# Kernel optimization log

Measured on AMD Instinct MI355X. Metric: run time of the kernel, lower is better.

## Reference

```python
import jax, jax.numpy as jnp
import numpy as np

EPS = 1e-5


def conv3x3(x, w, b):
    # x [B,C,H,W], w [O,C,3,3], stride 1, pad 1
    y = jax.lax.conv_general_dilated(x, w, (1, 1), ((1, 1), (1, 1)),
                                     dimension_numbers=('NCHW', 'OIHW', 'NCHW'))
    return y + b[None, :, None, None]


def bilinear_gather(x, py, px):
    # x [B,C,H,W]; sampling locations py,px [B,K,H,W] -> [B,C,K,H,W]
    # Zero padding outside the image (matches deform_conv CUDA semantics:
    # out-of-bound corner values contribute 0).
    B, C, H, W = x.shape
    K = py.shape[1]
    x_flat = x.reshape(B, C, H * W)
    y0 = jnp.floor(py)
    x0 = jnp.floor(px)
    out = jnp.zeros((B, C, K, H, W), x.dtype)
    for dy in (0.0, 1.0):
        for dx in (0.0, 1.0):
            yi = y0 + dy
            xi = x0 + dx
            wgt = (1.0 - jnp.abs(py - yi)) * (1.0 - jnp.abs(px - xi))  # [B,K,H,W]
            valid = (yi >= 0) & (yi <= H - 1) & (xi >= 0) & (xi <= W - 1)
            idx = (jnp.clip(yi, 0, H - 1).astype(jnp.int32) * W
                   + jnp.clip(xi, 0, W - 1).astype(jnp.int32)).reshape(B, -1)
            vals = jax.vmap(lambda xf, i: xf[:, i])(x_flat, idx)  # [B,C,K*H*W]
            out = out + (wgt * valid)[:, None] * vals.reshape(B, C, K, H, W)
    return out


def setup_inputs() -> dict:
    key = jax.random.key(0)
    k1, k2, k3 = jax.random.split(key, 3)
    B, C, O, H, W = 4, 64, 64, 128, 128
    x = jax.random.normal(k1, (B, C, H, W), jnp.float32)
    # offset predictor: small init so predicted offsets are modest (realistic)
    off_w = 0.01 * jax.random.normal(k2, (18, C, 3, 3), jnp.float32)
    off_b = jnp.zeros((18,), jnp.float32)
    dc_w = jax.random.normal(k3, (O, C, 3, 3), jnp.float32) / np.sqrt(C * 9)
    dc_b = jnp.zeros((O,), jnp.float32)
    gamma = jnp.ones((O,), jnp.float32)
    beta = jnp.zeros((O,), jnp.float32)
    return {"x": x, "off_w": off_w, "off_b": off_b, "dc_w": dc_w,
            "dc_b": dc_b, "gamma": gamma, "beta": beta}


def reference(x, off_w, off_b, dc_w, dc_b, gamma, beta):
    B, C, H, W = x.shape
    O = dc_w.shape[0]
    K = 9  # 3x3 kernel
    offset = conv3x3(x, off_w, off_b)              # [B,18,H,W]
    off = offset.reshape(B, K, 2, H, W)            # (dy,dx) per kernel tap, row-major
    dyo, dxo = off[:, :, 0], off[:, :, 1]          # [B,K,H,W]
    k = (jnp.arange(3) - 1).astype(x.dtype)        # kernel taps {-1,0,1}
    kgy = jnp.repeat(k, 3)                         # [9] row-major y offsets
    kgx = jnp.tile(k, 3)                           # [9] row-major x offsets
    hh = jnp.arange(H, dtype=x.dtype)
    ww = jnp.arange(W, dtype=x.dtype)
    # stride 1, pad 1: base point = out_pos - 1 + tap; pad is folded into kgy/kgx
    py = hh[None, None, :, None] + kgy[None, :, None, None] + dyo
    px = ww[None, None, None, :] + kgx[None, :, None, None] + dxo
    sampled = bilinear_gather(x, py, px)           # [B,C,K,H,W]
    y = jnp.einsum('ock,bckhw->bohw', dc_w.reshape(O, C, K), sampled)
    y = y + dc_b[None, :, None, None]
    # BatchNorm2d (training mode: biased batch statistics)
    mu = y.mean(axis=(0, 2, 3), keepdims=True)
    var = y.var(axis=(0, 2, 3), keepdims=True)
    yn = (y - mu) * jax.lax.rsqrt(var + EPS)
    return jax.nn.relu(yn * gamma[None, :, None, None] + beta[None, :, None, None])
```

## Files before the change

kernel.cpp:

```cpp
#include <hip/hip_runtime.h>

#define HH 128
#define WW 128
#define HWSZ (HH * WW)
#define CC 64
#define OO 64
#define BB 4
#define NOFF 18
#define KK 576

#define WS_BG     0
#define WS_BGO    18432
#define WS_SUMS   27648
#define WS_SUMSQ  27712
#define WS_YBUF   27776

typedef __attribute__((ext_vector_type(8))) short short8;
typedef __attribute__((ext_vector_type(4))) int int4v;
typedef __attribute__((ext_vector_type(2))) unsigned int uint2v;
typedef __attribute__((ext_vector_type(4))) float f32x4;

__device__ inline unsigned bf16rne(float f) {
  unsigned u = __float_as_uint(f);
  u += 0x7fff + ((u >> 16) & 1);
  return u >> 16;
}

__global__ __launch_bounds__(256) void prep_kernel(
    const float* __restrict__ x, const float* __restrict__ off_w,
    const float* __restrict__ dc_w, unsigned int* __restrict__ xTu,
    int* __restrict__ Bg, int* __restrict__ Bgo, float* __restrict__ sums) {
  int bid = blockIdx.x;
  if (bid < BB * HH) {
    __shared__ float T[CC][WW + 1];
    int b = bid >> 7, h = bid & 127;
    int tw = threadIdx.x & 127, th = threadIdx.x >> 7;
    const float* xp = x + (size_t)b * CC * HWSZ + h * WW;
#pragma unroll 8
    for (int i = 0; i < 32; ++i) {
      int c = i * 2 + th;
      T[c][tw] = xp[c * HWSZ + tw];
    }
    __syncthreads();
    int c2 = threadIdx.x & 31, wq = threadIdx.x >> 5;
    unsigned int* op = xTu + ((size_t)(b * HH + h) * WW) * 32;
#pragma unroll 8
    for (int i = 0; i < 16; ++i) {
      int w = i * 8 + wq;
      unsigned pk = bf16rne(T[2 * c2][w]) | (bf16rne(T[2 * c2 + 1][w]) << 16);
      op[w * 32 + c2] = pk;
    }
  } else {
    int pb = bid - BB * HH;
    int tid = pb * 256 + threadIdx.x;
    int stride = 64 * 256;
    for (int i = tid; i < 72 * 64 * 4; i += stride) {
      int j = i & 3, o = (i >> 2) & 63, g = i >> 8;
      int k2 = g * 4 + j, t = k2 >> 5, jj = k2 & 31;
      unsigned lo = bf16rne(dc_w[o * KK + (2 * jj) * 9 + t]);
      unsigned hi = bf16rne(dc_w[o * KK + (2 * jj + 1) * 9 + t]);
      Bg[i] = (int)(lo | (hi << 16));
    }
    for (int i = tid; i < 72 * 32 * 4; i += stride) {
      int j = i & 3, o = (i >> 2) & 31, g = i >> 7;
      int k2 = g * 4 + j, t = k2 >> 5, jj = k2 & 31;
      unsigned pk = 0;
      if (o < NOFF) {
        unsigned lo = bf16rne(off_w[o * KK + (2 * jj) * 9 + t]);
        unsigned hi = bf16rne(off_w[o * KK + (2 * jj + 1) * 9 + t]);
        pk = lo | (hi << 16);
      }
      Bgo[i] = (int)pk;
    }
    if (tid < 128) sums[tid] = 0.0f;
  }
}

#define G_ISSUE(i, T, PH)                                                     \
  int4v m##i, da##i, db##i, dcv##i, dd##i;                                    \
  {                                                                           \
    m##i = *(const int4v*)&Mw[(((PH) * 8 + p8) * 9 + (T)) * 4];               \
    unsigned x_ = (unsigned)m##i.x, y_ = (unsigned)m##i.y;                    \
    da##i  = *(const int4v*)&xbu[(x_ & 0xffffu) * 32 + cq4];                  \
    db##i  = *(const int4v*)&xbu[(x_ >> 16) * 32 + cq4];                      \
    dcv##i = *(const int4v*)&xbu[(y_ & 0xffffu) * 32 + cq4];                  \
    dd##i  = *(const int4v*)&xbu[(y_ >> 16) * 32 + cq4];                      \
  }

#define G_BLEND(i, T, PH)                                                     \
  {                                                                           \
    float w00_ = __uint_as_float(((unsigned)m##i.z) << 16);                   \
    float w01_ = __uint_as_float(((unsigned)m##i.z) & 0xffff0000u);           \
    float w10_ = __uint_as_float(((unsigned)m##i.w) << 16);                   \
    float w11_ = __uint_as_float(((unsigned)m##i.w) & 0xffff0000u);           \
    int4v pk_;                                                                \
    _Pragma("unroll")                                                         \
    for (int j = 0; j < 4; ++j) {                                             \
      float slo_ = w00_ * __uint_as_float(((unsigned)da##i[j]) << 16);        \
      slo_ = fmaf(w01_, __uint_as_float(((unsigned)db##i[j]) << 16), slo_);   \
      slo_ = fmaf(w10_, __uint_as_float(((unsigned)dcv##i[j]) << 16), slo_);  \
      slo_ = fmaf(w11_, __uint_as_float(((unsigned)dd##i[j]) << 16), slo_);   \
      float shi_ = w00_ * __uint_as_float(((unsigned)da##i[j]) & 0xffff0000u);\
      shi_ = fmaf(w01_, __uint_as_float(((unsigned)db##i[j]) & 0xffff0000u), shi_);\
      shi_ = fmaf(w10_, __uint_as_float(((unsigned)dcv##i[j]) & 0xffff0000u), shi_);\
      shi_ = fmaf(w11_, __uint_as_float(((unsigned)dd##i[j]) & 0xffff0000u), shi_);\
      pk_[j] = (int)__builtin_amdgcn_perm(__float_as_uint(shi_) + 0x8000u,    \
                                          __float_as_uint(slo_) + 0x8000u,    \
                                          0x07060302u);                       \
    }                                                                         \
    *(int4v*)&A[abase + ((T) & 1) * 544 + ((PH) * 8 + p8) * 34 + cq4] = pk_;  \
  }

#define MFMA_TAP(T)                                                           \
  {                                                                           \
    _Pragma("unroll")                                                         \
    for (int kk2 = 0; kk2 < 2; ++kk2) {                                       \
      int4v av = *(const int4v*)&A[abase + ((T) & 1) * 544 + n16 * 34 + kk2 * 16 + q * 4]; \
      short8 af = __builtin_bit_cast(short8, av);                             \
      int g = (T) * 8 + kk2 * 4 + q;                                          \
      _Pragma("unroll")                                                       \
      for (int nt = 0; nt < 4; ++nt) {                                        \
        int4v bv = *(const int4v*)&Bg[(g * 64 + nt * 16 + n16) * 4];          \
        short8 bfr = __builtin_bit_cast(short8, bv);                          \
        acc[nt] = __builtin_amdgcn_mfma_f32_16x16x32_bf16(af, bfr, acc[nt], 0, 0, 0); \
      }                                                                       \
    }                                                                         \
  }

__global__ __launch_bounds__(256, 6) void fused_kernel(
    const unsigned int* __restrict__ xTu, const int* __restrict__ Bg,
    const int* __restrict__ Bgo, const float* __restrict__ off_b,
    const float* __restrict__ dc_b, unsigned int* __restrict__ ybuf,
    float* __restrict__ part) {
  __shared__ __align__(16) int A[4 * 1088];
  __shared__ __align__(16) int M[4 * 144 * 4];

  int cg = threadIdx.x >> 6, lane = threadIdx.x & 63;
  int b = blockIdx.x >> 8, rem = blockIdx.x & 255;
  int h = rem >> 1, w0 = (rem & 1) * 64;
  int hw0 = h * WW + w0;
  int p0 = cg * 16;
  int abase = cg * 1088;
  int n16 = lane & 15, q = lane >> 4;
  int pg = lane >> 3, part8 = lane & 7;
  const unsigned int* xbu = xTu + (size_t)b * HWSZ * 32;

  f32x4 acc2[2] = {f32x4{0, 0, 0, 0}, f32x4{0, 0, 0, 0}};
#pragma unroll
  for (int t = 0; t < 9; ++t) {
    int ky = t / 3 - 1, kx = t % 3 - 1;
    int cy = h + ky;
    bool vy = (cy >= 0) && (cy < HH);
    int cys = min(max(cy, 0), HH - 1);
    int tb = abase + (t & 1) * 544;
#pragma unroll
    for (int i = 0; i < 2; ++i) {
      int px = i * 8 + pg;
      int cx = w0 + p0 + px + kx;
      bool v = vy && (cx >= 0) && (cx < WW);
      int cxs = min(max(cx, 0), WW - 1);
      int4v val = *(const int4v*)&xbu[(cys * WW + cxs) * 32 + part8 * 4];
      if (!v) { val.x = 0; val.y = 0; val.z = 0; val.w = 0; }
      *(int4v*)&A[tb + px * 34 + part8 * 4] = val;
    }
#pragma unroll
    for (int kk2 = 0; kk2 < 2; ++kk2) {
      int4v av = *(const int4v*)&A[tb + n16 * 34 + kk2 * 16 + q * 4];
      short8 af = __builtin_bit_cast(short8, av);
      int g = t * 8 + kk2 * 4 + q;
#pragma unroll
      for (int nt = 0; nt < 2; ++nt) {
        int4v bv = *(const int4v*)&Bgo[(g * 32 + nt * 16 + n16) * 4];
        short8 bfr = __builtin_bit_cast(short8, bv);
        acc2[nt] = __builtin_amdgcn_mfma_f32_16x16x32_bf16(af, bfr, acc2[nt], 0, 0, 0);
      }
    }
  }
  float* offLw = (float*)&A[abase];
#pragma unroll
  for (int nt = 0; nt < 2; ++nt) {
    int o = nt * 16 + n16;
    if (o < NOFF) {
      float bv = off_b[o];
#pragma unroll
      for (int r = 0; r < 4; ++r) offLw[o * 16 + q * 4 + r] = acc2[nt][r] + bv;
    }
  }

  int* Mw = M + cg * 144 * 4;
#pragma unroll
  for (int it = 0; it < 3; ++it) {
    int m = it * 64 + lane;
    if (m < 144) {
      int pxl = (unsigned)m / 9u;
      int t = m - pxl * 9;
      float dy = offLw[(2 * t) * 16 + pxl];
      float dx = offLw[(2 * t + 1) * 16 + pxl];
      float py = (float)(h + t / 3 - 1) + dy;
      float pxf = (float)(w0 + p0 + pxl + (t % 3) - 1) + dx;
      float fy0 = floorf(py), fx0 = floorf(pxf);
      float ay = py - fy0, ax = pxf - fx0;
      int iy0 = (int)fy0, ix0 = (int)fx0;
      int iy1 = iy0 + 1, ix1 = ix0 + 1;
      float wy0 = 1.0f - ay, wy1 = ay, wx0 = 1.0f - ax, wx1 = ax;
      if (!(iy0 >= 0 && iy0 < HH)) wy0 = 0.0f;
      if (!(iy1 >= 0 && iy1 < HH)) wy1 = 0.0f;
      if (!(ix0 >= 0 && ix0 < WW)) wx0 = 0.0f;
      if (!(ix1 >= 0 && ix1 < WW)) wx1 = 0.0f;
      int cy0 = min(max(iy0, 0), HH - 1), cy1 = min(max(iy1, 0), HH - 1);
      int cx0 = min(max(ix0, 0), WW - 1), cx1 = min(max(ix1, 0), WW - 1);
      int4v mv;
      mv.x = (cy0 * WW + cx0) | ((cy0 * WW + cx1) << 16);
      mv.y = (cy1 * WW + cx0) | ((cy1 * WW + cx1) << 16);
      mv.z = (int)(bf16rne(wy0 * wx0) | (bf16rne(wy0 * wx1) << 16));
      mv.w = (int)(bf16rne(wy1 * wx0) | (bf16rne(wy1 * wx1) << 16));
      *(int4v*)&Mw[m * 4] = mv;
    }
  }

  int p8 = lane >> 3;
  int cq4 = (lane & 7) * 4;
  f32x4 acc[4] = {f32x4{0,0,0,0}, f32x4{0,0,0,0}, f32x4{0,0,0,0}, f32x4{0,0,0,0}};
  G_ISSUE(0, 0, 0)   G_ISSUE(1, 0, 1)
  G_ISSUE(2, 1, 0)   G_ISSUE(3, 1, 1)   G_BLEND(0, 0, 0)   G_BLEND(1, 0, 1)   MFMA_TAP(0)
  G_ISSUE(4, 2, 0)   G_ISSUE(5, 2, 1)   G_BLEND(2, 1, 0)   G_BLEND(3, 1, 1)   MFMA_TAP(1)
  G_ISSUE(6, 3, 0)   G_ISSUE(7, 3, 1)   G_BLEND(4, 2, 0)   G_BLEND(5, 2, 1)   MFMA_TAP(2)
  G_ISSUE(8, 4, 0)   G_ISSUE(9, 4, 1)   G_BLEND(6, 3, 0)   G_BLEND(7, 3, 1)   MFMA_TAP(3)
  G_ISSUE(10, 5, 0)  G_ISSUE(11, 5, 1)  G_BLEND(8, 4, 0)   G_BLEND(9, 4, 1)   MFMA_TAP(4)
  G_ISSUE(12, 6, 0)  G_ISSUE(13, 6, 1)  G_BLEND(10, 5, 0)  G_BLEND(11, 5, 1)  MFMA_TAP(5)
  G_ISSUE(14, 7, 0)  G_ISSUE(15, 7, 1)  G_BLEND(12, 6, 0)  G_BLEND(13, 6, 1)  MFMA_TAP(6)
  G_ISSUE(16, 8, 0)  G_ISSUE(17, 8, 1)  G_BLEND(14, 7, 0)  G_BLEND(15, 7, 1)  MFMA_TAP(7)
  G_BLEND(16, 8, 0)  G_BLEND(17, 8, 1)  MFMA_TAP(8)

  float* SW = (float*)&A[abase];
#pragma unroll
  for (int nt = 0; nt < 4; ++nt) {
    int o = nt * 16 + n16;
    float bv = dc_b[o];
    f32x4 r;
    float s = 0.0f, ss = 0.0f;
#pragma unroll
    for (int r0 = 0; r0 < 4; ++r0) {
      r[r0] = acc[nt][r0] + bv;
      s += r[r0];
      ss += r[r0] * r[r0];
    }
    unsigned pk0 = __builtin_amdgcn_perm(__float_as_uint(r[1]) + 0x8000u,
                                         __float_as_uint(r[0]) + 0x8000u,
                                         0x07060302u);
    unsigned pk1 = __builtin_amdgcn_perm(__float_as_uint(r[3]) + 0x8000u,
                                         __float_as_uint(r[2]) + 0x8000u,
                                         0x07060302u);
    uint2v pk; pk.x = pk0; pk.y = pk1;
    *(uint2v*)&ybuf[(size_t)(b * OO + o) * (HWSZ / 2) + ((hw0 + p0) >> 1) + q * 2] = pk;
    s += __shfl_xor(s, 16);  s += __shfl_xor(s, 32);
    ss += __shfl_xor(ss, 16); ss += __shfl_xor(ss, 32);
    if (lane < 16) {
      SW[nt * 16 + lane] = s;
      SW[64 + nt * 16 + lane] = ss;
    }
  }
  __syncthreads();
  if (threadIdx.x < 64) {
    float ts = 0.0f, tq = 0.0f;
#pragma unroll
    for (int wv = 0; wv < 4; ++wv) {
      const float* Sv = (const float*)&A[wv * 1088];
      ts += Sv[threadIdx.x];
      tq += Sv[64 + threadIdx.x];
    }
    part[(size_t)blockIdx.x * 128 + threadIdx.x] = ts;
    part[(size_t)blockIdx.x * 128 + 64 + threadIdx.x] = tq;
  }
}

__global__ __launch_bounds__(64) void reduce_kernel(
    const float* __restrict__ part, float* __restrict__ sums) {
  int t = blockIdx.x;
  int j = threadIdx.x;
  float s = 0.0f;
#pragma unroll
  for (int k = 0; k < 16; ++k) s += part[(size_t)(j + 64 * k) * 128 + t];
#pragma unroll
  for (int off = 32; off > 0; off >>= 1) s += __shfl_down(s, off);
  if (j == 0) sums[t] = s;
}

__global__ __launch_bounds__(256) void norm_kernel(
    const unsigned int* __restrict__ ybuf, const float* __restrict__ sums,
    const float* __restrict__ sumsq, const float* __restrict__ gamma,
    const float* __restrict__ beta, float* __restrict__ out) {
  int gid = blockIdx.x * 256 + threadIdx.x;
  int flat = gid << 2;
  int o = (flat >> 14) & 63;
  const float invN = 1.0f / (float)(BB * HWSZ);
  float mean = sums[o] * invN;
  float var = sumsq[o] * invN - mean * mean;
  float rstd = rsqrtf(var + 1e-5f);
  float g = gamma[o] * rstd;
  float bta = beta[o] - mean * g;
  uint2v v = ((const uint2v*)ybuf)[gid];
  float4 r;
  r.x = fmaxf(__uint_as_float(v.x << 16) * g + bta, 0.0f);
  r.y = fmaxf(__uint_as_float(v.x & 0xffff0000u) * g + bta, 0.0f);
  r.z = fmaxf(__uint_as_float(v.y << 16) * g + bta, 0.0f);
  r.w = fmaxf(__uint_as_float(v.y & 0xffff0000u) * g + bta, 0.0f);
  ((float4*)out)[gid] = r;
}

extern "C" void kernel_launch(void* const* d_in, const int* in_sizes, int n_in,
                              void* d_out, int out_size, void* d_ws, size_t ws_size,
                              hipStream_t stream) {
  const float* x     = (const float*)d_in[0];
  const float* off_w = (const float*)d_in[1];
  const float* off_b = (const float*)d_in[2];
  const float* dc_w  = (const float*)d_in[3];
  const float* dc_b  = (const float*)d_in[4];
  const float* gamma = (const float*)d_in[5];
  const float* beta  = (const float*)d_in[6];
  float* ws = (float*)d_ws;
  int*   Bg     = (int*)(ws + WS_BG);
  int*   Bgo    = (int*)(ws + WS_BGO);
  float* sums   = ws + WS_SUMS;
  float* sumsq  = ws + WS_SUMSQ;
  unsigned int* ybuf = (unsigned int*)(ws + WS_YBUF);
  float* out = (float*)d_out;
  unsigned int* xTu = (unsigned int*)d_out;
  float* part = (float*)d_out + 2097152;

  prep_kernel<<<BB * HH + 64, 256, 0, stream>>>(x, off_w, dc_w, xTu, Bg, Bgo, sums);
  fused_kernel<<<BB * HWSZ / 64, 256, 0, stream>>>(xTu, Bg, Bgo, off_b, dc_b, ybuf, part);
  reduce_kernel<<<128, 64, 0, stream>>>(part, sums);
  norm_kernel<<<BB * OO * HWSZ / (4 * 256), 256, 0, stream>>>(ybuf, sums, sumsq, gamma, beta, out);
}
```

Before: 125.3 us.

## Fuse BN statistics reduction into normalize kernel and vectorize prep transpose loads

Removes the separate reduce kernel: each normalize block now re-reduces the per-block partial sums and sums of squares for its channel via wave shuffles and shared memory. Partials move from the output buffer to workspace. The prep transpose loads x with float4 reads. This saves a launch but adds redundant, strided partial reads in every normalize block.

```diff
diff --git a/kernel.cpp b/kernel.cpp
--- a/kernel.cpp
+++ b/kernel.cpp
@@ -11,9 +11,8 @@
 
 #define WS_BG     0
 #define WS_BGO    18432
-#define WS_SUMS   27648
-#define WS_SUMSQ  27712
 #define WS_YBUF   27776
+#define WS_PART   2125952
 
 typedef __attribute__((ext_vector_type(8))) short short8;
 typedef __attribute__((ext_vector_type(4))) int int4v;
@@ -29,17 +28,22 @@
 __global__ __launch_bounds__(256) void prep_kernel(
     const float* __restrict__ x, const float* __restrict__ off_w,
     const float* __restrict__ dc_w, unsigned int* __restrict__ xTu,
-    int* __restrict__ Bg, int* __restrict__ Bgo, float* __restrict__ sums) {
+    int* __restrict__ Bg, int* __restrict__ Bgo) {
   int bid = blockIdx.x;
   if (bid < BB * HH) {
     __shared__ float T[CC][WW + 1];
     int b = bid >> 7, h = bid & 127;
-    int tw = threadIdx.x & 127, th = threadIdx.x >> 7;
     const float* xp = x + (size_t)b * CC * HWSZ + h * WW;
-#pragma unroll 8
-    for (int i = 0; i < 32; ++i) {
-      int c = i * 2 + th;
-      T[c][tw] = xp[c * HWSZ + tw];
+    int j = threadIdx.x;
+#pragma unroll
+    for (int i = 0; i < 8; ++i) {
+      int l = i * 256 + j;
+      int c = l >> 5, w4 = l & 31;
+      float4 v = *(const float4*)(xp + (size_t)c * HWSZ + w4 * 4);
+      T[c][w4 * 4 + 0] = v.x;
+      T[c][w4 * 4 + 1] = v.y;
+      T[c][w4 * 4 + 2] = v.z;
+      T[c][w4 * 4 + 3] = v.w;
     }
     __syncthreads();
     int c2 = threadIdx.x & 31, wq = threadIdx.x >> 5;
@@ -72,7 +76,6 @@
       }
       Bgo[i] = (int)pk;
     }
-    if (tid < 128) sums[tid] = 0.0f;
   }
 }
 
@@ -274,28 +277,37 @@
   }
 }
 
-__global__ __launch_bounds__(64) void reduce_kernel(
-    const float* __restrict__ part, float* __restrict__ sums) {
-  int t = blockIdx.x;
+__global__ __launch_bounds__(256) void norm_kernel(
+    const unsigned int* __restrict__ ybuf, const float* __restrict__ part,
+    const float* __restrict__ gamma, const float* __restrict__ beta,
+    float* __restrict__ out) {
+  __shared__ float red[16];
+  int gid = blockIdx.x * 256 + threadIdx.x;
+  int o = ((blockIdx.x * 1024) >> 14) & 63;
   int j = threadIdx.x;
-  float s = 0.0f;
-#pragma unroll
-  for (int k = 0; k < 16; ++k) s += part[(size_t)(j + 64 * k) * 128 + t];
-#pragma unroll
-  for (int off = 32; off > 0; off >>= 1) s += __shfl_down(s, off);
-  if (j == 0) sums[t] = s;
-}
-
-__global__ __launch_bounds__(256) void norm_kernel(
-    const unsigned int* __restrict__ ybuf, const float* __restrict__ sums,
-    const float* __restrict__ sumsq, const float* __restrict__ gamma,
-    const float* __restrict__ beta, float* __restrict__ out) {
-  int gid = blockIdx.x * 256 + threadIdx.x;
-  int flat = gid << 2;
-  int o = (flat >> 14) & 63;
+  float s = 0.0f, sq = 0.0f;
+#pragma unroll
+  for (int k = 0; k < 4; ++k) {
+    s  += part[(size_t)(j + 256 * k) * 128 + o];
+    sq += part[(size_t)(j + 256 * k) * 128 + 64 + o];
+  }
+#pragma unroll
+  for (int off = 1; off < 64; off <<= 1) {
+    s += __shfl_xor(s, off);
+    sq += __shfl_xor(sq, off);
+  }
+  if ((threadIdx.x & 63) == 0) {
+    int w = threadIdx.x >> 6;
+    red[w] = s;
+    red[8 + w] = sq;
+  }
+  __syncthreads();
+  float sm = red[0] + red[1] + red[2] + red[3];
+  float sqq = red[8] + red[9] + red[10] + red[11];
+
   const float invN = 1.0f / (float)(BB * HWSZ);
-  float mean = sums[o] * invN;
-  float var = sumsq[o] * invN - mean * mean;
+  float mean = sm * invN;
+  float var = sqq * invN - mean * mean;
   float rstd = rsqrtf(var + 1e-5f);
   float g = gamma[o] * rstd;
   float bta = beta[o] - mean * g;
@@ -321,15 +333,12 @@
   float* ws = (float*)d_ws;
   int*   Bg     = (int*)(ws + WS_BG);
   int*   Bgo    = (int*)(ws + WS_BGO);
-  float* sums   = ws + WS_SUMS;
-  float* sumsq  = ws + WS_SUMSQ;
   unsigned int* ybuf = (unsigned int*)(ws + WS_YBUF);
+  float* part   = ws + WS_PART;
   float* out = (float*)d_out;
   unsigned int* xTu = (unsigned int*)d_out;
-  float* part = (float*)d_out + 2097152;
-
-  prep_kernel<<<BB * HH + 64, 256, 0, stream>>>(x, off_w, dc_w, xTu, Bg, Bgo, sums);
+
+  prep_kernel<<<BB * HH + 64, 256, 0, stream>>>(x, off_w, dc_w, xTu, Bg, Bgo);
   fused_kernel<<<BB * HWSZ / 64, 256, 0, stream>>>(xTu, Bg, Bgo, off_b, dc_b, ybuf, part);
-  reduce_kernel<<<128, 64, 0, stream>>>(part, sums);
-  norm_kernel<<<BB * OO * HWSZ / (4 * 256), 256, 0, stream>>>(ybuf, sums, sumsq, gamma, beta, out);
-}
+  norm_kernel<<<BB * OO * HWSZ / (4 * 256), 256, 0, stream>>>(ybuf, part, gamma, beta, out);
+}
```

New measurement: 146.0 us. +16.4%, slower.
